# Optimization experiments

Hardware: AMD Instinct MI355X
Metric: run time of the kernel (lower is better)

## Reference

```python
import jax, jax.numpy as jnp
import numpy as np

N_CLASSES = 10
NBD_PAD = 1
EPS = 1e-5  # nn.LayerNorm default eps


def _neighbor_states(state, n):
    # state: [B, n_classes, H, W]; replicates F.unfold(kernel=2n+1, padding=n)
    # then drops the center tap. Kernel positions enumerated row-major, matching
    # unfold's (C, K2) channel ordering after the view in the torch code.
    B, C, H, W = state.shape
    k = 2 * n + 1
    center = (k * k) // 2
    padded = jnp.pad(state, ((0, 0), (0, 0), (n, n), (n, n)))
    shifts = []
    for idx in range(k * k):
        if idx == center:
            continue
        ki, kj = divmod(idx, k)
        shifts.append(padded[:, :, ki:ki + H, kj:kj + W])
    nb = jnp.stack(shifts, axis=2)  # [B, C, K2-1, H, W]
    return nb.reshape(B, C * (k * k - 1), H, W)


def setup_inputs() -> dict:
    key = jax.random.key(0)
    ks = jax.random.split(key, 7)
    B, C, H, W = 64, 32, 128, 128
    NN_HID, PERC = 128, 112
    x = jax.random.normal(ks[0], (B, C, H, W), dtype=jnp.float32)
    w1 = jax.random.normal(ks[1], (NN_HID, PERC), dtype=jnp.float32) * (1.0 / np.sqrt(PERC))
    b1 = jax.random.normal(ks[2], (NN_HID,), dtype=jnp.float32) * 0.02
    w2 = jax.random.normal(ks[3], (C, NN_HID), dtype=jnp.float32) * (1.0 / np.sqrt(NN_HID))
    b2 = jax.random.normal(ks[4], (C,), dtype=jnp.float32) * 0.02
    gamma = jnp.ones((C,), dtype=jnp.float32) + 0.1 * jax.random.normal(ks[5], (C,), dtype=jnp.float32)
    beta = 0.1 * jax.random.normal(ks[6], (C,), dtype=jnp.float32)
    return {"x": x, "w1": w1, "b1": b1, "w2": w2, "b2": b2, "gamma": gamma, "beta": beta}


def reference(x, w1, b1, w2, b2, gamma, beta):
    # perceive: [B, in_ch + n_classes*(K2-1), H, W]
    nb = _neighbor_states(x[:, :N_CLASSES], NBD_PAD)
    perc = jnp.concatenate([x, nb], axis=1)
    # 1x1 conv MLP (fire_rate == 1.0 -> no update mask)
    h = jax.nn.relu(jnp.einsum('bchw,oc->bohw', perc, w1) + b1[None, :, None, None])
    dx = jnp.einsum('bchw,oc->bohw', h, w2) + b2[None, :, None, None]
    new_state = x + dx
    # clean_slate_if_white: zero hidden channels where argmax class == 0 (no_grad mask)
    pred = jnp.argmax(new_state[:, :N_CLASSES], axis=1)  # [B,H,W]
    inv = jax.lax.stop_gradient((pred != 0).astype(new_state.dtype))[:, None]  # [B,1,H,W]
    new_state = jnp.concatenate(
        [new_state[:, :N_CLASSES], new_state[:, N_CLASSES:] * inv], axis=1)
    # LayerNorm over channel dim (torch permutes to NHWC, norms last dim, permutes back)
    mu = jnp.mean(new_state, axis=1, keepdims=True)
    var = jnp.var(new_state, axis=1, keepdims=True)
    xn = (new_state - mu) * jax.lax.rsqrt(var + EPS)
    return xn * gamma[None, :, None, None] + beta[None, :, None, None]
```

## Files before the change

kernel.cpp:

```cpp
#include <hip/hip_runtime.h>

typedef unsigned short U16;
typedef unsigned int U32;
typedef __bf16 bf16;
typedef bf16 bf16x8 __attribute__((ext_vector_type(8)));
typedef U16  u16x8  __attribute__((ext_vector_type(8)));
typedef float f32x4 __attribute__((ext_vector_type(4)));

__device__ __forceinline__ void split3(float a, U16& o1, U16& o2, U16& o3) {
    U32 ua = __float_as_uint(a);
    float a1 = __uint_as_float(ua & 0xFFFF0000u);
    float r1 = a - a1;
    U32 u2 = __float_as_uint(r1);
    float a2 = __uint_as_float(u2 & 0xFFFF0000u);
    float r2 = r1 - a2;
    o1 = (U16)(ua >> 16);
    o2 = (U16)(u2 >> 16);
    o3 = (U16)(__float_as_uint(r2) >> 16);
}

__device__ __forceinline__ void split3x8(const float v[8], bf16x8& A1, bf16x8& A2, bf16x8& A3) {
    u16x8 e1, e2, e3;
    #pragma unroll
    for (int j = 0; j < 8; ++j) { U16 a, b, c; split3(v[j], a, b, c); e1[j] = a; e2[j] = b; e3[j] = c; }
    A1 = __builtin_bit_cast(bf16x8, e1);
    A2 = __builtin_bit_cast(bf16x8, e2);
    A3 = __builtin_bit_cast(bf16x8, e3);
}


__global__ __launch_bounds__(256, 2)
void cann_kernel(const float* __restrict__ xg,  const float* __restrict__ w1g,
                 const float* __restrict__ b1g, const float* __restrict__ w2g,
                 const float* __restrict__ b2g, const float* __restrict__ gg,
                 const float* __restrict__ bg,  float* __restrict__ outg)
{
    __shared__ __align__(16) unsigned char smem[33792 + 3 * 8704];
    float* sPf   = (float*)smem;
    U16*   sW2L0 = (U16*)(smem + 33792);
    U16*   sW2L1 = (U16*)(smem + 33792 + 8704);
    U16*   sW2L2 = (U16*)(smem + 33792 + 2 * 8704);
    float* dxl   = (float*)(smem + 33792);

    const int tid  = threadIdx.x;
    const int bid  = blockIdx.x;
    const int jseg = bid & 1;
    const int irow = (bid >> 1) & 127;
    const int b    = bid >> 8;
    const int jbase = jseg << 6;

    const int lane = tid & 63;
    const int wv   = tid >> 6;
    const int quad = lane >> 4;
    const int col  = lane & 15;

    {
        int c  = tid >> 3;
        int j8 = (tid & 7) << 3;
        const float* src = xg + (b * 32 + c) * 16384 + irow * 128 + jbase + j8;
        float4 v0 = *(const float4*)src;
        float4 v1 = *(const float4*)(src + 4);
        sPf[(j8 + 0) * 132 + c] = v0.x;  sPf[(j8 + 1) * 132 + c] = v0.y;
        sPf[(j8 + 2) * 132 + c] = v0.z;  sPf[(j8 + 3) * 132 + c] = v0.w;
        sPf[(j8 + 4) * 132 + c] = v1.x;  sPf[(j8 + 5) * 132 + c] = v1.y;
        sPf[(j8 + 6) * 132 + c] = v1.z;  sPf[(j8 + 7) * 132 + c] = v1.w;

        #pragma unroll
        for (int pass = 0; pass < 5; ++pass) {
            int j   = tid + pass * 256;
            int ch  = j >> 4;
            int p4  = (j & 15) << 2;
            int cls = ch >> 3, t = ch & 7;
            int di = (int)((0x22211000u >> (4 * t)) & 0xFu) - 1;
            int dj = (int)((0x21020210u >> (4 * t)) & 0xFu) - 1;
            int row = irow + di;
            bool rok = (unsigned)row < 128u;
            const float* base = xg + (b * 32 + cls) * 16384 + row * 128;
            int cb = jbase + p4 + dj;
            #pragma unroll
            for (int r = 0; r < 4; ++r) {
                int cc = cb + r;
                float v = (rok && (unsigned)cc < 128u) ? base[cc] : 0.0f;
                sPf[(p4 + r) * 132 + 32 + ch] = v;
            }
        }
        #pragma unroll
        for (int q = 0; q < 4; ++q) {
            int idx = tid + q * 256;
            int p = idx >> 4, cc = idx & 15;
            sPf[p * 132 + 112 + cc] = 0.0f;
        }
        int n  = tid >> 3;
        int k0 = (tid & 7) << 4;
        const float* ws = w2g + n * 128 + k0;
        U16 t1[16], t2[16], t3[16];
        #pragma unroll
        for (int e = 0; e < 16; ++e) split3(ws[e], t1[e], t2[e], t3[e]);
        #define PK(t, e) ((U32)t[e] | ((U32)t[(e)+1] << 16))
        {
            uint4 q0 = make_uint4(PK(t1,0), PK(t1,2), PK(t1,4), PK(t1,6));
            uint4 q1 = make_uint4(PK(t1,8), PK(t1,10), PK(t1,12), PK(t1,14));
            *(uint4*)(sW2L0 + n * 136 + k0) = q0; *(uint4*)(sW2L0 + n * 136 + k0 + 8) = q1;
            q0 = make_uint4(PK(t2,0), PK(t2,2), PK(t2,4), PK(t2,6));
            q1 = make_uint4(PK(t2,8), PK(t2,10), PK(t2,12), PK(t2,14));
            *(uint4*)(sW2L1 + n * 136 + k0) = q0; *(uint4*)(sW2L1 + n * 136 + k0 + 8) = q1;
            q0 = make_uint4(PK(t3,0), PK(t3,2), PK(t3,4), PK(t3,6));
            q1 = make_uint4(PK(t3,8), PK(t3,10), PK(t3,12), PK(t3,14));
            *(uint4*)(sW2L2 + n * 136 + k0) = q0; *(uint4*)(sW2L2 + n * 136 + k0 + 8) = q1;
        }
        #undef PK
    }

    bf16x8 bw1[3][2][4];
    #pragma unroll
    for (int n2 = 0; n2 < 2; ++n2)
        #pragma unroll
        for (int ks = 0; ks < 4; ++ks) {
            int n  = wv * 32 + n2 * 16 + col;
            int k0 = ks * 32 + quad * 8;
            float v[8];
            if (k0 < 112) {
                const float* s = w1g + n * 112 + k0;
                float4 a = *(const float4*)s;
                float4 c = *(const float4*)(s + 4);
                v[0] = a.x; v[1] = a.y; v[2] = a.z; v[3] = a.w;
                v[4] = c.x; v[5] = c.y; v[6] = c.z; v[7] = c.w;
            } else {
                #pragma unroll
                for (int j = 0; j < 8; ++j) v[j] = 0.0f;
            }
            split3x8(v, bw1[0][n2][ks], bw1[1][n2][ks], bw1[2][n2][ks]);
        }
    const float b1v0 = b1g[wv * 32 + col];
    const float b1v1 = b1g[wv * 32 + 16 + col];
    const float b2v0 = b2g[col];
    const float b2v1 = b2g[16 + col];

    __syncthreads();

    float xs[2][4];
    #pragma unroll
    for (int n2 = 0; n2 < 2; ++n2)
        #pragma unroll
        for (int r = 0; r < 4; ++r)
            xs[n2][r] = sPf[(wv * 16 + quad * 4 + r) * 132 + n2 * 16 + col];

    const f32x4 fz = {0.f, 0.f, 0.f, 0.f};
    f32x4 acc1[4][2];
    #pragma unroll
    for (int mt = 0; mt < 4; ++mt) { acc1[mt][0] = fz; acc1[mt][1] = fz; }

    #pragma unroll
    for (int mt = 0; mt < 4; ++mt) {
        const float* ap = &sPf[(mt * 16 + col) * 132];
        #pragma unroll
        for (int ks = 0; ks < 4; ++ks) {
            int k0 = ks * 32 + quad * 8;
            float v[8];
            float4 lo = *(const float4*)(ap + k0);
            float4 hi = *(const float4*)(ap + k0 + 4);
            v[0] = lo.x; v[1] = lo.y; v[2] = lo.z; v[3] = lo.w;
            v[4] = hi.x; v[5] = hi.y; v[6] = hi.z; v[7] = hi.w;
            bf16x8 A1, A2, A3;
            split3x8(v, A1, A2, A3);
            #pragma unroll
            for (int n2 = 0; n2 < 2; ++n2) {
                f32x4 a = acc1[mt][n2];
                a = __builtin_amdgcn_mfma_f32_16x16x32_bf16(A1, bw1[0][n2][ks], a, 0, 0, 0);
                a = __builtin_amdgcn_mfma_f32_16x16x32_bf16(A1, bw1[1][n2][ks], a, 0, 0, 0);
                a = __builtin_amdgcn_mfma_f32_16x16x32_bf16(A2, bw1[0][n2][ks], a, 0, 0, 0);
                a = __builtin_amdgcn_mfma_f32_16x16x32_bf16(A1, bw1[2][n2][ks], a, 0, 0, 0);
                a = __builtin_amdgcn_mfma_f32_16x16x32_bf16(A2, bw1[1][n2][ks], a, 0, 0, 0);
                a = __builtin_amdgcn_mfma_f32_16x16x32_bf16(A3, bw1[0][n2][ks], a, 0, 0, 0);
                acc1[mt][n2] = a;
            }
        }
    }
    __syncthreads();

    #pragma unroll
    for (int mt = 0; mt < 4; ++mt)
        #pragma unroll
        for (int n2 = 0; n2 < 2; ++n2) {
            float bb = n2 ? b1v1 : b1v0;
            #pragma unroll
            for (int r = 0; r < 4; ++r)
                sPf[(mt * 16 + quad * 4 + r) * 132 + wv * 32 + n2 * 16 + col] =
                    fmaxf(acc1[mt][n2][r] + bb, 0.0f);
        }
    __syncthreads();

    f32x4 acc2[2];
    acc2[0] = fz; acc2[1] = fz;
    {
        const float* hp = &sPf[(wv * 16 + col) * 132];
        #pragma unroll
        for (int ks = 0; ks < 4; ++ks) {
            int k0 = ks * 32 + quad * 8;
            float v[8];
            float4 lo = *(const float4*)(hp + k0);
            float4 hi = *(const float4*)(hp + k0 + 4);
            v[0] = lo.x; v[1] = lo.y; v[2] = lo.z; v[3] = lo.w;
            v[4] = hi.x; v[5] = hi.y; v[6] = hi.z; v[7] = hi.w;
            bf16x8 H1, H2, H3;
            split3x8(v, H1, H2, H3);
            #pragma unroll
            for (int n2 = 0; n2 < 2; ++n2) {
                int boff = (n2 * 16 + col) * 136 + k0;
                bf16x8 B1 = *(const bf16x8*)&sW2L0[boff];
                bf16x8 B2 = *(const bf16x8*)&sW2L1[boff];
                bf16x8 B3 = *(const bf16x8*)&sW2L2[boff];
                f32x4 a = acc2[n2];
                a = __builtin_amdgcn_mfma_f32_16x16x32_bf16(H1, B1, a, 0, 0, 0);
                a = __builtin_amdgcn_mfma_f32_16x16x32_bf16(H1, B2, a, 0, 0, 0);
                a = __builtin_amdgcn_mfma_f32_16x16x32_bf16(H2, B1, a, 0, 0, 0);
                a = __builtin_amdgcn_mfma_f32_16x16x32_bf16(H1, B3, a, 0, 0, 0);
                a = __builtin_amdgcn_mfma_f32_16x16x32_bf16(H2, B2, a, 0, 0, 0);
                a = __builtin_amdgcn_mfma_f32_16x16x32_bf16(H3, B1, a, 0, 0, 0);
                acc2[n2] = a;
            }
        }
    }
    __syncthreads();

    #pragma unroll
    for (int n2 = 0; n2 < 2; ++n2) {
        float bb = n2 ? b2v1 : b2v0;
        int c = n2 * 16 + col;
        #pragma unroll
        for (int r = 0; r < 4; ++r) {
            int p = wv * 16 + quad * 4 + r;
            dxl[p * 33 + c] = acc2[n2][r] + bb + xs[n2][r];
        }
    }
    __syncthreads();

    if (tid < 64) {
        int p = tid;
        float ns[32];
        #pragma unroll
        for (int c = 0; c < 32; ++c) ns[c] = dxl[p * 33 + c];
        float m = ns[1];
        #pragma unroll
        for (int c = 2; c < 10; ++c) m = fmaxf(m, ns[c]);
        float keep = (m > ns[0]) ? 1.0f : 0.0f;
        #pragma unroll
        for (int c = 10; c < 32; ++c) ns[c] *= keep;
        float s = 0.f;
        #pragma unroll
        for (int c = 0; c < 32; ++c) s += ns[c];
        float mu = s * 0.03125f;
        float var = 0.f;
        #pragma unroll
        for (int c = 0; c < 32; ++c) { float d = ns[c] - mu; var += d * d; }
        var *= 0.03125f;
        float rstd = 1.0f / sqrtf(var + 1e-5f);
        int base = b * 524288 + irow * 128 + jbase + p;
        #pragma unroll
        for (int c = 0; c < 32; ++c) {
            outg[base + c * 16384] = (ns[c] - mu) * rstd * gg[c] + bg[c];
        }
    }
}

extern "C" void kernel_launch(void* const* d_in, const int* in_sizes, int n_in,
                              void* d_out, int out_size, void* d_ws, size_t ws_size,
                              hipStream_t stream) {
    const float* x  = (const float*)d_in[0];
    const float* w1 = (const float*)d_in[1];
    const float* b1 = (const float*)d_in[2];
    const float* w2 = (const float*)d_in[3];
    const float* b2 = (const float*)d_in[4];
    const float* g  = (const float*)d_in[5];
    const float* be = (const float*)d_in[6];
    float* out = (float*)d_out;
    hipLaunchKernelGGL(cann_kernel, dim3(16384), dim3(256), 0, stream,
                       x, w1, b1, w2, b2, g, be, out);
}
```

Measured before the change: 588.9 us.

## Pre-split weights into bf16 triples in a prep kernel and store split activations in LDS

Adds a small prep kernel that splits w1 and w2 into three bf16 limbs once and writes them to workspace. The main kernel then loads these pre-split weights from global memory instead of re-splitting them in every block. Activations and hidden values are split once when written to shared memory as bf16 limbs, rather than being re-split from fp32 on each MFMA operand load. This shrinks LDS use and raises launch bounds to 3 blocks per SM. The costs are an extra launch and the w2 operands for the second GEMM now coming from global or L2 rather than LDS.

```diff
diff --git a/kernel.cpp b/kernel.cpp
--- a/kernel.cpp
+++ b/kernel.cpp
@@ -28,19 +28,41 @@
     A3 = __builtin_bit_cast(bf16x8, e3);
 }
 
-
-__global__ __launch_bounds__(256, 2)
-void cann_kernel(const float* __restrict__ xg,  const float* __restrict__ w1g,
-                 const float* __restrict__ b1g, const float* __restrict__ w2g,
-                 const float* __restrict__ b2g, const float* __restrict__ gg,
-                 const float* __restrict__ bg,  float* __restrict__ outg)
+__global__ __launch_bounds__(256)
+void prep_kernel(const float* __restrict__ w1g, const float* __restrict__ w2g,
+                 U16* __restrict__ w1L, U16* __restrict__ w2L)
 {
-    __shared__ __align__(16) unsigned char smem[33792 + 3 * 8704];
-    float* sPf   = (float*)smem;
-    U16*   sW2L0 = (U16*)(smem + 33792);
-    U16*   sW2L1 = (U16*)(smem + 33792 + 8704);
-    U16*   sW2L2 = (U16*)(smem + 33792 + 2 * 8704);
-    float* dxl   = (float*)(smem + 33792);
+    int tid = blockIdx.x * 256 + threadIdx.x;
+    if (tid < 2048) {
+        int n = tid >> 4, k0 = (tid & 15) << 3;
+        float v[8];
+        #pragma unroll
+        for (int j = 0; j < 8; ++j) { int k = k0 + j; v[j] = (k < 112) ? w1g[n * 112 + k] : 0.0f; }
+        bf16x8 L1, L2, L3; split3x8(v, L1, L2, L3);
+        *(bf16x8*)(w1L + 0 * 16384 + n * 128 + k0) = L1;
+        *(bf16x8*)(w1L + 1 * 16384 + n * 128 + k0) = L2;
+        *(bf16x8*)(w1L + 2 * 16384 + n * 128 + k0) = L3;
+    }
+    if (tid < 512) {
+        int n = tid >> 4, k0 = (tid & 15) << 3;
+        float v[8];
+        #pragma unroll
+        for (int j = 0; j < 8; ++j) v[j] = w2g[n * 128 + k0 + j];
+        bf16x8 L1, L2, L3; split3x8(v, L1, L2, L3);
+        *(bf16x8*)(w2L + 0 * 4096 + n * 128 + k0) = L1;
+        *(bf16x8*)(w2L + 1 * 4096 + n * 128 + k0) = L2;
+        *(bf16x8*)(w2L + 2 * 4096 + n * 128 + k0) = L3;
+    }
+}
+
+__global__ __launch_bounds__(256, 3)
+void cann_kernel(const float* __restrict__ xg,  const U16* __restrict__ w1L,
+                 const U16* __restrict__ w2L,
+                 const float* __restrict__ b1g, const float* __restrict__ b2g,
+                 const float* __restrict__ gg,  const float* __restrict__ bg,
+                 float* __restrict__ outg)
+{
+    __shared__ __align__(16) U16 sL[3 * 8704];
 
     const int tid  = threadIdx.x;
     const int bid  = blockIdx.x;
@@ -48,67 +70,54 @@
     const int irow = (bid >> 1) & 127;
     const int b    = bid >> 8;
     const int jbase = jseg << 6;
-
     const int lane = tid & 63;
     const int wv   = tid >> 6;
     const int quad = lane >> 4;
     const int col  = lane & 15;
 
     {
-        int c  = tid >> 3;
-        int j8 = (tid & 7) << 3;
-        const float* src = xg + (b * 32 + c) * 16384 + irow * 128 + jbase + j8;
-        float4 v0 = *(const float4*)src;
-        float4 v1 = *(const float4*)(src + 4);
-        sPf[(j8 + 0) * 132 + c] = v0.x;  sPf[(j8 + 1) * 132 + c] = v0.y;
-        sPf[(j8 + 2) * 132 + c] = v0.z;  sPf[(j8 + 3) * 132 + c] = v0.w;
-        sPf[(j8 + 4) * 132 + c] = v1.x;  sPf[(j8 + 5) * 132 + c] = v1.y;
-        sPf[(j8 + 6) * 132 + c] = v1.z;  sPf[(j8 + 7) * 132 + c] = v1.w;
-
-        #pragma unroll
-        for (int pass = 0; pass < 5; ++pass) {
-            int j   = tid + pass * 256;
-            int ch  = j >> 4;
-            int p4  = (j & 15) << 2;
-            int cls = ch >> 3, t = ch & 7;
-            int di = (int)((0x22211000u >> (4 * t)) & 0xFu) - 1;
-            int dj = (int)((0x21020210u >> (4 * t)) & 0xFu) - 1;
-            int row = irow + di;
-            bool rok = (unsigned)row < 128u;
-            const float* base = xg + (b * 32 + cls) * 16384 + row * 128;
-            int cb = jbase + p4 + dj;
-            #pragma unroll
-            for (int r = 0; r < 4; ++r) {
-                int cc = cb + r;
-                float v = (rok && (unsigned)cc < 128u) ? base[cc] : 0.0f;
-                sPf[(p4 + r) * 132 + 32 + ch] = v;
+        int px = tid & 63;
+        int cg = tid >> 6;
+        const float* src = xg + (b * 32 + cg * 8) * 16384 + irow * 128 + jbase + px;
+        float v[8];
+        #pragma unroll
+        for (int i = 0; i < 8; ++i) v[i] = src[i * 16384];
+        bf16x8 L1, L2, L3; split3x8(v, L1, L2, L3);
+        int o = px * 136 + cg * 8;
+        *(bf16x8*)&sL[o] = L1;
+        *(bf16x8*)&sL[8704 + o] = L2;
+        *(bf16x8*)&sL[17408 + o] = L3;
+
+        #pragma unroll
+        for (int pass = 0; pass < 3; ++pass) {
+            int j = tid + pass * 256;
+            if (j < 640) {
+                int tpx = j & 63, cls = j >> 6;
+                const float* cbase = xg + (b * 32 + cls) * 16384;
+                float tv[8];
+                #pragma unroll
+                for (int t = 0; t < 8; ++t) {
+                    int di = (int)((0x22211000u >> (4 * t)) & 0xFu) - 1;
+                    int dj = (int)((0x21020210u >> (4 * t)) & 0xFu) - 1;
+                    int row = irow + di;
+                    int cc  = jbase + tpx + dj;
+                    tv[t] = ((unsigned)row < 128u && (unsigned)cc < 128u)
+                            ? cbase[row * 128 + cc] : 0.0f;
+                }
+                bf16x8 T1, T2, T3; split3x8(tv, T1, T2, T3);
+                int to = tpx * 136 + 32 + cls * 8;
+                *(bf16x8*)&sL[to] = T1;
+                *(bf16x8*)&sL[8704 + to] = T2;
+                *(bf16x8*)&sL[17408 + to] = T3;
             }
         }
-        #pragma unroll
-        for (int q = 0; q < 4; ++q) {
-            int idx = tid + q * 256;
-            int p = idx >> 4, cc = idx & 15;
-            sPf[p * 132 + 112 + cc] = 0.0f;
-        }
-        int n  = tid >> 3;
-        int k0 = (tid & 7) << 4;
-        const float* ws = w2g + n * 128 + k0;
-        U16 t1[16], t2[16], t3[16];
-        #pragma unroll
-        for (int e = 0; e < 16; ++e) split3(ws[e], t1[e], t2[e], t3[e]);
-        #define PK(t, e) ((U32)t[e] | ((U32)t[(e)+1] << 16))
-        {
-            uint4 q0 = make_uint4(PK(t1,0), PK(t1,2), PK(t1,4), PK(t1,6));
-            uint4 q1 = make_uint4(PK(t1,8), PK(t1,10), PK(t1,12), PK(t1,14));
-            *(uint4*)(sW2L0 + n * 136 + k0) = q0; *(uint4*)(sW2L0 + n * 136 + k0 + 8) = q1;
-            q0 = make_uint4(PK(t2,0), PK(t2,2), PK(t2,4), PK(t2,6));
-            q1 = make_uint4(PK(t2,8), PK(t2,10), PK(t2,12), PK(t2,14));
-            *(uint4*)(sW2L1 + n * 136 + k0) = q0; *(uint4*)(sW2L1 + n * 136 + k0 + 8) = q1;
-            q0 = make_uint4(PK(t3,0), PK(t3,2), PK(t3,4), PK(t3,6));
-            q1 = make_uint4(PK(t3,8), PK(t3,10), PK(t3,12), PK(t3,14));
-            *(uint4*)(sW2L2 + n * 136 + k0) = q0; *(uint4*)(sW2L2 + n * 136 + k0 + 8) = q1;
-        }
-        #undef PK
+        if (tid < 128) {
+            int zo = (tid >> 1) * 136 + 112 + (tid & 1) * 8;
+            uint4 z = make_uint4(0u, 0u, 0u, 0u);
+            *(uint4*)&sL[zo] = z;
+            *(uint4*)&sL[8704 + zo] = z;
+            *(uint4*)&sL[17408 + zo] = z;
+        }
     }
 
     bf16x8 bw1[3][2][4];
@@ -118,32 +127,24 @@
         for (int ks = 0; ks < 4; ++ks) {
             int n  = wv * 32 + n2 * 16 + col;
             int k0 = ks * 32 + quad * 8;
-            float v[8];
-            if (k0 < 112) {
-                const float* s = w1g + n * 112 + k0;
-                float4 a = *(const float4*)s;
-                float4 c = *(const float4*)(s + 4);
-                v[0] = a.x; v[1] = a.y; v[2] = a.z; v[3] = a.w;
-                v[4] = c.x; v[5] = c.y; v[6] = c.z; v[7] = c.w;
-            } else {
-                #pragma unroll
-                for (int j = 0; j < 8; ++j) v[j] = 0.0f;
-            }
-            split3x8(v, bw1[0][n2][ks], bw1[1][n2][ks], bw1[2][n2][ks]);
+            #pragma unroll
+            for (int L = 0; L < 3; ++L)
+                bw1[L][n2][ks] = *(const bf16x8*)(w1L + L * 16384 + n * 128 + k0);
         }
     const float b1v0 = b1g[wv * 32 + col];
     const float b1v1 = b1g[wv * 32 + 16 + col];
     const float b2v0 = b2g[col];
     const float b2v1 = b2g[16 + col];
 
-    __syncthreads();
-
     float xs[2][4];
     #pragma unroll
     for (int n2 = 0; n2 < 2; ++n2)
         #pragma unroll
         for (int r = 0; r < 4; ++r)
-            xs[n2][r] = sPf[(wv * 16 + quad * 4 + r) * 132 + n2 * 16 + col];
+            xs[n2][r] = xg[(b * 32 + n2 * 16 + col) * 16384 + irow * 128 + jbase
+                           + wv * 16 + quad * 4 + r];
+
+    __syncthreads();
 
     const f32x4 fz = {0.f, 0.f, 0.f, 0.f};
     f32x4 acc1[4][2];
@@ -152,17 +153,12 @@
 
     #pragma unroll
     for (int mt = 0; mt < 4; ++mt) {
-        const float* ap = &sPf[(mt * 16 + col) * 132];
         #pragma unroll
         for (int ks = 0; ks < 4; ++ks) {
-            int k0 = ks * 32 + quad * 8;
-            float v[8];
-            float4 lo = *(const float4*)(ap + k0);
-            float4 hi = *(const float4*)(ap + k0 + 4);
-            v[0] = lo.x; v[1] = lo.y; v[2] = lo.z; v[3] = lo.w;
-            v[4] = hi.x; v[5] = hi.y; v[6] = hi.z; v[7] = hi.w;
-            bf16x8 A1, A2, A3;
-            split3x8(v, A1, A2, A3);
+            int ao = (mt * 16 + col) * 136 + ks * 32 + quad * 8;
+            bf16x8 A1 = *(const bf16x8*)&sL[ao];
+            bf16x8 A2 = *(const bf16x8*)&sL[8704 + ao];
+            bf16x8 A3 = *(const bf16x8*)&sL[17408 + ao];
             #pragma unroll
             for (int n2 = 0; n2 < 2; ++n2) {
                 f32x4 a = acc1[mt][n2];
@@ -184,45 +180,43 @@
         for (int n2 = 0; n2 < 2; ++n2) {
             float bb = n2 ? b1v1 : b1v0;
             #pragma unroll
-            for (int r = 0; r < 4; ++r)
-                sPf[(mt * 16 + quad * 4 + r) * 132 + wv * 32 + n2 * 16 + col] =
-                    fmaxf(acc1[mt][n2][r] + bb, 0.0f);
+            for (int r = 0; r < 4; ++r) {
+                float v = fmaxf(acc1[mt][n2][r] + bb, 0.0f);
+                U16 u1, u2, u3; split3(v, u1, u2, u3);
+                int ho = (mt * 16 + quad * 4 + r) * 136 + wv * 32 + n2 * 16 + col;
+                sL[ho] = u1; sL[8704 + ho] = u2; sL[17408 + ho] = u3;
+            }
         }
     __syncthreads();
 
     f32x4 acc2[2];
     acc2[0] = fz; acc2[1] = fz;
-    {
-        const float* hp = &sPf[(wv * 16 + col) * 132];
-        #pragma unroll
-        for (int ks = 0; ks < 4; ++ks) {
-            int k0 = ks * 32 + quad * 8;
-            float v[8];
-            float4 lo = *(const float4*)(hp + k0);
-            float4 hi = *(const float4*)(hp + k0 + 4);
-            v[0] = lo.x; v[1] = lo.y; v[2] = lo.z; v[3] = lo.w;
-            v[4] = hi.x; v[5] = hi.y; v[6] = hi.z; v[7] = hi.w;
-            bf16x8 H1, H2, H3;
-            split3x8(v, H1, H2, H3);
-            #pragma unroll
-            for (int n2 = 0; n2 < 2; ++n2) {
-                int boff = (n2 * 16 + col) * 136 + k0;
-                bf16x8 B1 = *(const bf16x8*)&sW2L0[boff];
-                bf16x8 B2 = *(const bf16x8*)&sW2L1[boff];
-                bf16x8 B3 = *(const bf16x8*)&sW2L2[boff];
-                f32x4 a = acc2[n2];
-                a = __builtin_amdgcn_mfma_f32_16x16x32_bf16(H1, B1, a, 0, 0, 0);
-                a = __builtin_amdgcn_mfma_f32_16x16x32_bf16(H1, B2, a, 0, 0, 0);
-                a = __builtin_amdgcn_mfma_f32_16x16x32_bf16(H2, B1, a, 0, 0, 0);
-                a = __builtin_amdgcn_mfma_f32_16x16x32_bf16(H1, B3, a, 0, 0, 0);
-                a = __builtin_amdgcn_mfma_f32_16x16x32_bf16(H2, B2, a, 0, 0, 0);
-                a = __builtin_amdgcn_mfma_f32_16x16x32_bf16(H3, B1, a, 0, 0, 0);
-                acc2[n2] = a;
-            }
-        }
-    }
-    __syncthreads();
-
+    #pragma unroll
+    for (int ks = 0; ks < 4; ++ks) {
+        int k0 = ks * 32 + quad * 8;
+        int ho = (wv * 16 + col) * 136 + k0;
+        bf16x8 H1 = *(const bf16x8*)&sL[ho];
+        bf16x8 H2 = *(const bf16x8*)&sL[8704 + ho];
+        bf16x8 H3 = *(const bf16x8*)&sL[17408 + ho];
+        #pragma unroll
+        for (int n2 = 0; n2 < 2; ++n2) {
+            int bo = (n2 * 16 + col) * 128 + k0;
+            bf16x8 B1 = *(const bf16x8*)(w2L + 0 * 4096 + bo);
+            bf16x8 B2 = *(const bf16x8*)(w2L + 1 * 4096 + bo);
+            bf16x8 B3 = *(const bf16x8*)(w2L + 2 * 4096 + bo);
+            f32x4 a = acc2[n2];
+            a = __builtin_amdgcn_mfma_f32_16x16x32_bf16(H1, B1, a, 0, 0, 0);
+            a = __builtin_amdgcn_mfma_f32_16x16x32_bf16(H1, B2, a, 0, 0, 0);
+            a = __builtin_amdgcn_mfma_f32_16x16x32_bf16(H2, B1, a, 0, 0, 0);
+            a = __builtin_amdgcn_mfma_f32_16x16x32_bf16(H1, B3, a, 0, 0, 0);
+            a = __builtin_amdgcn_mfma_f32_16x16x32_bf16(H2, B2, a, 0, 0, 0);
+            a = __builtin_amdgcn_mfma_f32_16x16x32_bf16(H3, B1, a, 0, 0, 0);
+            acc2[n2] = a;
+        }
+    }
+    __syncthreads();
+
+    float* dxl = (float*)sL;
     #pragma unroll
     for (int n2 = 0; n2 < 2; ++n2) {
         float bb = n2 ? b2v1 : b2v0;
@@ -257,9 +251,8 @@
         float rstd = 1.0f / sqrtf(var + 1e-5f);
         int base = b * 524288 + irow * 128 + jbase + p;
         #pragma unroll
-        for (int c = 0; c < 32; ++c) {
+        for (int c = 0; c < 32; ++c)
             outg[base + c * 16384] = (ns[c] - mu) * rstd * gg[c] + bg[c];
-        }
     }
 }
 
@@ -274,6 +267,11 @@
     const float* g  = (const float*)d_in[5];
     const float* be = (const float*)d_in[6];
     float* out = (float*)d_out;
+
+    U16* w1L = (U16*)d_ws;
+    U16* w2L = (U16*)((char*)d_ws + 98304);
+
+    hipLaunchKernelGGL(prep_kernel, dim3(8), dim3(256), 0, stream, w1, w2, w1L, w2L);
     hipLaunchKernelGGL(cann_kernel, dim3(16384), dim3(256), 0, stream,
-                       x, w1, b1, w2, b2, g, be, out);
-}
+                       x, w1L, w2L, b1, b2, g, be, out);
+}
```

Measured after the change: 583.4 us. Within noise of the previous version (-0.9%).
